# Optimization experiments

Hardware: AMD Instinct MI355X
Metric: run time of the kernel (lower is better)

Reference implementation:

```python
import jax, jax.numpy as jnp
import numpy as np
import jax.scipy.linalg as jsp

H = 8
C = 64
D_CONV = 4
EPS_L2 = 1e-6
EPS_RMS = 1e-5


def l2norm(x):
    return x * jax.lax.rsqrt(jnp.sum(x * x, axis=-1, keepdims=True) + EPS_L2)


def setup_inputs() -> dict:
    key = jax.random.key(0)
    ks = jax.random.split(key, 12)
    B, T, D = 4, 4096, 1024
    x = jax.random.normal(ks[0], (B, T, D), dtype=jnp.float32)
    s = 0.02
    Wv = jax.random.normal(ks[1], (D, D), dtype=jnp.float32) * s
    Wg = jax.random.normal(ks[2], (D, D), dtype=jnp.float32) * s
    Wo = jax.random.normal(ks[3], (D, D), dtype=jnp.float32) * s
    Wb = jax.random.normal(ks[4], (H, D), dtype=jnp.float32) * s
    Wa = jax.random.normal(ks[5], (H, D), dtype=jnp.float32) * s
    # dt_bias / A_log initialized as in the torch module
    u = jax.random.uniform(ks[6], (H,))
    dt = jnp.exp(u * (jnp.log(0.1) - jnp.log(0.001)) + jnp.log(0.001))
    dt_bias = dt + jnp.log(-jnp.expm1(-dt))
    A_log = jnp.log(jax.random.uniform(ks[7], (H,)) * 16.0 + 1e-4)
    norm_w = jnp.ones((D // H,), dtype=jnp.float32)
    conv_w = jax.random.normal(ks[8], (D, D_CONV), dtype=jnp.float32) * 0.1
    conv_b = jnp.zeros((D,), dtype=jnp.float32)
    return {"x": x, "Wv": Wv, "Wg": Wg, "Wo": Wo, "Wb": Wb, "Wa": Wa,
            "dt_bias": dt_bias, "A_log": A_log, "norm_w": norm_w,
            "conv_w": conv_w, "conv_b": conv_b}


def _causal_depthwise_conv(x, w, b):
    # x: (B,T,D), w: (D,d_conv) -- causal depthwise conv1d
    B, T, D = x.shape
    xp = jnp.pad(x, ((0, 0), (D_CONV - 1, 0), (0, 0)))
    out = b
    for j in range(D_CONV):
        out = out + xp[:, j:j + T] * w[:, j]
    return out


def _forward(x, Wv, Wg, Wo, Wb, Wa, dt_bias, A_log, norm_w, conv_w, conv_b):
    B, T, D = x.shape
    K = D // H
    n = T // C  # T chosen as a multiple of C, so pad_len == 0

    rk = l2norm(x.reshape(B, T, H, K)) / np.sqrt(K)
    x_shift = jnp.pad(x[:, :-1], ((0, 0), (1, 0), (0, 0)))
    wk = l2norm(x_shift.reshape(B, T, H, K))
    v = jax.nn.silu(_causal_depthwise_conv(x @ Wv.T, conv_w, conv_b)).reshape(B, T, H, K)
    gate = (x @ Wg.T).reshape(B, T, H, K)
    beta = jax.nn.sigmoid(x @ Wb.T)                       # (B,T,H)
    decay = -jnp.exp(A_log) * jax.nn.softplus(x @ Wa.T + dt_bias)  # (B,T,H)

    # -> (B,H,T,K)
    rk, wk, v = (jnp.transpose(t, (0, 2, 1, 3)) for t in (rk, wk, v))
    beta_t = jnp.transpose(beta, (0, 2, 1))[..., None]    # (B,H,T,1)
    v = v * beta_t
    wk_beta = wk * beta_t

    # chunk: (B,H,n,C,K)
    ch = lambda t: t.reshape(B, H, n, C, K)
    rk, wk, v, wk_beta = ch(rk), ch(wk), ch(v), ch(wk_beta)
    decay = jnp.cumsum(jnp.transpose(decay, (0, 2, 1)).reshape(B, H, n, C), axis=-1)
    decay_exp = jnp.exp(decay)[..., None]                 # (B,H,n,C,1)

    tril = jnp.tril(jnp.ones((C, C), dtype=bool))
    strict_lower = jnp.tril(jnp.ones((C, C), dtype=bool), k=-1)
    diff = decay[..., :, None] - decay[..., None, :]
    L_mask = jnp.where(tril, jnp.exp(jnp.where(tril, diff, 0.0)), 0.0)  # (B,H,n,C,C)

    A_strict = jnp.where(strict_lower,
                         -(jnp.einsum('bhnck,bhndk->bhncd', wk_beta, wk) * L_mask), 0.0)
    # forward-substitution loop == inverse of unit-lower-triangular (I - A_strict)
    eye = jnp.eye(C, dtype=x.dtype)
    Tmat = jsp.solve_triangular(eye - A_strict,
                                jnp.broadcast_to(eye, A_strict.shape),
                                lower=True)
    v = Tmat @ v
    wk_cumdecay = Tmat @ (wk_beta * decay_exp)

    # scan over chunks maintaining state S: (B,H,K,K)
    def step(S, inp):
        rk_i, wk_i, v_i, wkc_i, L_i, dec_i = inp
        attn = jnp.where(tril, jnp.einsum('bhck,bhdk->bhcd', rk_i, wk_i) * L_i, 0.0)
        v_new = v_i - wkc_i @ S
        o_inter = (rk_i * jnp.exp(dec_i)[..., None]) @ S
        o_i = o_inter + attn @ v_new
        dw = jnp.exp(dec_i[..., -1:] - dec_i)[..., None]
        S_new = S * jnp.exp(dec_i[..., -1])[..., None, None] + \
            jnp.einsum('bhck,bhcv->bhkv', wk_i * dw, v_new)
        return S_new, o_i

    mv = lambda t: jnp.moveaxis(t, 2, 0)  # chunk axis to front
    S0 = jnp.zeros((B, H, K, K), dtype=x.dtype)
    _, o = jax.lax.scan(step, S0, (mv(rk), mv(wk), mv(v), mv(wk_cumdecay),
                                   mv(L_mask), mv(decay)))
    # o: (n,B,H,C,K) -> (B,T,H,K)
    o = jnp.transpose(o, (1, 0, 3, 2, 4)).reshape(B, T, H, K)

    # per-head RMSNorm, gated, output projection
    o = o * jax.lax.rsqrt(jnp.mean(o * o, axis=-1, keepdims=True) + EPS_RMS) * norm_w
    o = o * jax.nn.silu(gate)
    return o.reshape(B, T, D) @ Wo.T


def reference(x, Wv, Wg, Wo, Wb, Wa, dt_bias, A_log, norm_w, conv_w, conv_b):
    return _forward(x, Wv, Wg, Wo, Wb, Wa, dt_bias, A_log, norm_w, conv_w, conv_b)
```

## Files before the change

### kernel.cpp

```cpp
#include <hip/hip_runtime.h>
#include <hip/hip_bf16.h>
#include <math.h>

#define H_ 8
#define K_ 128
#define C_ 64
#define D_ 1024
#define T_ 4096
#define B_ 4
#define N_CH 64
#define BT_ (B_*T_)

typedef __attribute__((ext_vector_type(8))) short bf16x8;
typedef __attribute__((ext_vector_type(4))) float f32x4;
typedef __hip_bfloat16 bf16;

#define BAR_LGKM() do { \
  asm volatile("s_waitcnt lgkmcnt(0)" ::: "memory"); \
  __builtin_amdgcn_sched_barrier(0); \
  __builtin_amdgcn_s_barrier(); \
} while(0)

__device__ __forceinline__ float siluf(float x){ return x / (1.0f + expf(-x)); }
__device__ __forceinline__ float expn(float x){ return expf(fminf(x, 0.f)); }
__device__ __forceinline__ float sanf(float v){ return (__builtin_fabsf(v) <= 1e30f) ? v : 0.f; }

__device__ __forceinline__ void ld_bf4(const bf16* p, float* o){
  uint2 u = *(const uint2*)p;
  o[0]=__uint_as_float(u.x<<16); o[1]=__uint_as_float(u.x&0xffff0000u);
  o[2]=__uint_as_float(u.y<<16); o[3]=__uint_as_float(u.y&0xffff0000u);
}
__device__ __forceinline__ void ld_bf4s(const bf16* p, float* o){
  ld_bf4(p, o);
#pragma unroll
  for (int e=0;e<4;e++) o[e] = sanf(o[e]);
}
__device__ __forceinline__ unsigned short f2bfu(float f){
  bf16 h = __float2bfloat16(f);
  return *reinterpret_cast<unsigned short*>(&h);
}
__device__ __forceinline__ uint2 pack_bf4(const float* v){
  uint2 r;
  r.x = (unsigned)f2bfu(v[0]) | ((unsigned)f2bfu(v[1])<<16);
  r.y = (unsigned)f2bfu(v[2]) | ((unsigned)f2bfu(v[3])<<16);
  return r;
}
__device__ __forceinline__ bf16x8 u4_to_b8(uint4 u){
  union { uint4 u; bf16x8 b; } cv; cv.u = u; return cv.b;
}

template<int I> __device__ __forceinline__ void fsub_step(float* v, const float (*sa)[64]){
  const float* ar = sa[I];
  float s0=0.f,s1=0.f,s2=0.f,s3=0.f;
  constexpr int I4 = I & ~3;
#pragma unroll
  for (int j=0;j<I4;j+=4){
    float4 a4 = *(const float4*)&ar[j];
    s0 += a4.x*v[j+0]; s1 += a4.y*v[j+1]; s2 += a4.z*v[j+2]; s3 += a4.w*v[j+3];
  }
#pragma unroll
  for (int j=I4;j<I;j++) s0 += ar[j]*v[j];
  v[I] += (s0+s2)+(s1+s3);
}
template<int I> __device__ __forceinline__ void fsub_all(float* v, const float (*sa)[64]){
  if constexpr (I >= 1){
    fsub_all<I-1>(v, sa);
    fsub_step<I>(v, sa);
  }
}

__global__ __launch_bounds__(256) void cast_f2b(
    const float* __restrict__ src, bf16* __restrict__ dst, int n4)
{
  int i = blockIdx.x*256 + threadIdx.x;
  if (i >= n4) return;
  float4 v = *(const float4*)&src[(size_t)i*4];
  float a[4] = {v.x, v.y, v.z, v.w};
  *(uint2*)&dst[(size_t)i*4] = pack_bf4(a);
}

template<typename OUT_T, bool FUSE_NG>
__global__ __launch_bounds__(256) void gemm_bt_mfma(
    const bf16* __restrict__ X, const bf16* __restrict__ W,
    OUT_T* __restrict__ Y, int M, int N, int K,
    const bf16* __restrict__ o_in, const float* __restrict__ norm_w)
{
  __shared__ __align__(16) bf16 As[128*64];
  __shared__ __align__(16) bf16 Bs[128*64];
  const int tid = threadIdx.x;
  const int wv = tid >> 6;
  const int lane = tid & 63;
  const int row0 = blockIdx.y*128, col0 = blockIdx.x*128;
  const int mw = (wv&1)*64, nw = (wv>>1)*64;
  const int q = lane >> 4;
  const int l15 = lane & 15;
  const int swr = l15 & 7;
  f32x4 acc[4][4];
#pragma unroll
  for (int mi=0;mi<4;mi++)
#pragma unroll
    for (int ni=0;ni<4;ni++) acc[mi][ni] = (f32x4){0.f,0.f,0.f,0.f};

  const int sr8 = lane >> 3;
  const int scs = ((lane & 7) ^ sr8) * 8;
  for (int k0=0;k0<K;k0+=64){
#pragma unroll
    for (int i=0;i<4;i++){
      __builtin_amdgcn_global_load_lds(
          (const void*)&X[(size_t)(row0 + i*32 + wv*8 + sr8)*K + k0 + scs],
          (void*)&As[i*2048 + wv*512], 16, 0, 0);
      __builtin_amdgcn_global_load_lds(
          (const void*)&W[(size_t)(col0 + i*32 + wv*8 + sr8)*K + k0 + scs],
          (void*)&Bs[i*2048 + wv*512], 16, 0, 0);
    }
    __syncthreads();
#pragma unroll
    for (int ks=0; ks<64; ks+=32){
      bf16x8 af[4], bfr[4];
#pragma unroll
      for (int i=0;i<4;i++){
        const int cc = (((ks>>3) + q) ^ swr) * 8;
        af[i]  = *(const bf16x8*)&As[(mw + i*16 + l15)*64 + cc];
        bfr[i] = *(const bf16x8*)&Bs[(nw + i*16 + l15)*64 + cc];
      }
#pragma unroll
      for (int mi=0;mi<4;mi++)
#pragma unroll
        for (int ni=0;ni<4;ni++)
          acc[mi][ni] = __builtin_amdgcn_mfma_f32_16x16x32_bf16(af[mi], bfr[ni], acc[mi][ni], 0,0,0);
    }
    __syncthreads();
  }

  if constexpr (FUSE_NG){
    float* s_red = (float*)As;
    const int hh = blockIdx.x;
    const int nwh = nw >> 6;
#pragma unroll
    for (int mi=0;mi<4;mi++){
#pragma unroll
      for (int reg=0;reg<4;reg++){
        int row = row0 + mw + mi*16 + q*4 + reg;
        int b = row >> 12, t = row & (T_-1);
        const bf16* orow = o_in + ((size_t)(b*H_+hh)*T_ + t)*K_;
        float ps = 0.f;
#pragma unroll
        for (int ni=0;ni<4;ni++){
          float ov = sanf(__bfloat162float(orow[nw + ni*16 + l15]));
          ps += ov*ov;
        }
        ps += __shfl_xor(ps,1,64); ps += __shfl_xor(ps,2,64);
        ps += __shfl_xor(ps,4,64); ps += __shfl_xor(ps,8,64);
        if (l15 == 0) s_red[nwh*128 + mw + mi*16 + q*4 + reg] = ps;
      }
    }
    __syncthreads();
#pragma unroll
    for (int mi=0;mi<4;mi++){
#pragma unroll
      for (int reg=0;reg<4;reg++){
        int lr = mw + mi*16 + q*4 + reg;
        float ssum = s_red[lr] + s_red[128 + lr];
        float rr = rsqrtf(ssum*(1.f/128.f) + 1e-5f);
        int row = row0 + lr;
        int b = row >> 12, t = row & (T_-1);
        const bf16* orow = o_in + ((size_t)(b*H_+hh)*T_ + t)*K_;
#pragma unroll
        for (int ni=0;ni<4;ni++){
          int k = nw + ni*16 + l15;
          float ov = sanf(__bfloat162float(orow[k]));
          float res = ov * rr * norm_w[k] * siluf(acc[mi][ni][reg]);
          Y[(size_t)row*N + col0 + k] = (OUT_T)__float2bfloat16(res);
        }
      }
    }
  } else {
#pragma unroll
    for (int mi=0;mi<4;mi++){
#pragma unroll
      for (int reg=0;reg<4;reg++){
        int row = row0 + mw + mi*16 + q*4 + reg;
#pragma unroll
        for (int ni=0;ni<4;ni++){
          int col = col0 + nw + ni*16 + l15;
          if constexpr (sizeof(OUT_T) == 2)
            Y[(size_t)row*N + col] = (OUT_T)__float2bfloat16(acc[mi][ni][reg]);
          else
            Y[(size_t)row*N + col] = (OUT_T)acc[mi][ni][reg];
        }
      }
    }
  }
}

__global__ __launch_bounds__(256) void proj_small(
    const float* __restrict__ x, const float* __restrict__ Wb, const float* __restrict__ Wa,
    const float* __restrict__ dt_bias, const float* __restrict__ A_log,
    float* __restrict__ beta_out, float* __restrict__ dec_out)
{
  const int w = threadIdx.x >> 6;
  const int lane = threadIdx.x & 63;
  const int bt = blockIdx.x*4 + w;
  const int b = bt >> 12, t = bt & (T_-1);
  const float* xr = x + (size_t)bt*D_;
  float xv[16];
#pragma unroll
  for (int p=0;p<4;p++){
    float4 v = *(const float4*)&xr[lane*16 + p*4];
    xv[p*4+0]=v.x; xv[p*4+1]=v.y; xv[p*4+2]=v.z; xv[p*4+3]=v.w;
  }
  float accb[H_], acca[H_];
#pragma unroll
  for (int h=0;h<H_;h++){
    float sb=0.f, sa=0.f;
#pragma unroll
    for (int p=0;p<4;p++){
      float4 wb = *(const float4*)&Wb[(size_t)h*D_ + lane*16 + p*4];
      float4 wa = *(const float4*)&Wa[(size_t)h*D_ + lane*16 + p*4];
      sb += xv[p*4+0]*wb.x + xv[p*4+1]*wb.y + xv[p*4+2]*wb.z + xv[p*4+3]*wb.w;
      sa += xv[p*4+0]*wa.x + xv[p*4+1]*wa.y + xv[p*4+2]*wa.z + xv[p*4+3]*wa.w;
    }
    accb[h]=sb; acca[h]=sa;
  }
#pragma unroll
  for (int h=0;h<H_;h++){
#pragma unroll
    for (int m=1;m<64;m<<=1){
      accb[h] += __shfl_xor(accb[h], m, 64);
      acca[h] += __shfl_xor(acca[h], m, 64);
    }
  }
  if (lane < H_) {
    int h = lane;
    beta_out[(size_t)(b*H_+h)*T_ + t] = 1.f/(1.f+expf(-accb[h]));
  } else if (lane < 2*H_) {
    int h = lane - H_;
    float z = acca[h] + dt_bias[h];
    float sp = fmaxf(z,0.f) + log1pf(expf(-fabsf(z)));
    dec_out[(size_t)(b*H_+h)*T_ + t] = -expf(A_log[h]) * sp;
  }
}

__global__ __launch_bounds__(256) void xinv_kernel(
    const float* __restrict__ x, float* __restrict__ xinv, bf16* __restrict__ xb)
{
  const int bt = blockIdx.x;
  const int b = bt >> 12, t = bt & (T_-1);
  const int tid = threadIdx.x;
  float4 xv = *(const float4*)&x[(size_t)bt*D_ + tid*4];
  float a[4] = {xv.x, xv.y, xv.z, xv.w};
  *(uint2*)&xb[(size_t)bt*D_ + tid*4] = pack_bf4(a);
  float ss = xv.x*xv.x + xv.y*xv.y + xv.z*xv.z + xv.w*xv.w;
#pragma unroll
  for (int m=1;m<32;m<<=1) ss += __shfl_xor(ss, m, 32);
  const int h = tid >> 5;
  if ((tid & 31) == 0)
    xinv[(size_t)(b*H_+h)*T_ + t] = rsqrtf(ss + 1e-6f);
}

__global__ __launch_bounds__(256) void cumsum_dec(
    const float* __restrict__ dec_raw, float* __restrict__ dec_cum)
{
  int g = blockIdx.x*4 + (threadIdx.x>>6);
  int lane = threadIdx.x & 63;
  float v = sanf(dec_raw[(size_t)g*C_ + lane]);
#pragma unroll
  for (int off=1; off<64; off<<=1){
    float u = __shfl_up(v, off, 64);
    if (lane >= off) v += u;
  }
  dec_cum[(size_t)g*C_ + lane] = v;
}

__global__ __launch_bounds__(256) void chunk_prep(
    const bf16* __restrict__ xb, const float* __restrict__ xinv,
    const bf16* __restrict__ vpre, const float* __restrict__ cw, const float* __restrict__ cb,
    const float* __restrict__ beta, const float* __restrict__ dec,
    bf16* __restrict__ vchk, bf16* __restrict__ wkc, bf16* __restrict__ attn)
{
  __shared__ __align__(16) bf16 s_x[65][136];
  __shared__ __align__(16) float s_a[64][64];
  __shared__ float s_dec[64], s_beta[64], s_invsh[64], s_negbi[64], s_rsc[64], s_sc2[64];

  const int tid = threadIdx.x;
  const int chunk = blockIdx.x;
  const int bh = chunk >> 6;
  const int nc = chunk & 63;
  const int b = bh >> 3, h = bh & 7;
  const int t0 = nc * C_;
  const size_t xrow = (size_t)b*T_;
  const size_t rowb = (size_t)bh*T_ + t0;
  const size_t kobase = rowb * K_;
  const int w = tid >> 6;
  const int lane = tid & 63;
  const int l15 = lane & 15;
  const int q = lane >> 4;

  for (int idx = tid; idx < 65*16; idx += 256){
    int r = idx >> 4;
    int seg = (idx & 15) * 8;
    int t = t0 + r - 1;
    int tr = t < 0 ? 0 : t;
    *(uint4*)&s_x[r][seg] = *(const uint4*)&xb[(xrow + tr)*D_ + h*K_ + seg];
  }
  if (tid < C_){
    int c = tid;
    float dv  = sanf(dec[rowb + c]);
    float bet = sanf(beta[rowb + c]);
    float invc = sanf(xinv[rowb + c]);
    int tm1 = t0 + c - 1;
    float ivs = (tm1 >= 0) ? sanf(xinv[(size_t)bh*T_ + tm1]) : 0.f;
    s_dec[c] = dv;
    s_beta[c] = bet;
    s_invsh[c] = ivs;
    s_negbi[c] = -bet * ivs;
    s_rsc[c] = invc * 0.08838834764831845f;
    s_sc2[c] = ivs * bet * expn(dv);
  }
  __syncthreads();

  bf16x8 aG[4], aT[4];
#pragma unroll
  for (int ks=0; ks<4; ks++){
    aG[ks] = *(const bf16x8*)&s_x[16*w + l15][ks*32 + q*8];
    aT[ks] = *(const bf16x8*)&s_x[16*w + l15 + 1][ks*32 + q*8];
  }
  f32x4 accG[4], accT[4];
#pragma unroll
  for (int J=0;J<4;J++){ accG[J]=(f32x4){0.f,0.f,0.f,0.f}; accT[J]=(f32x4){0.f,0.f,0.f,0.f}; }
#pragma unroll
  for (int J=0;J<4;J++){
    if (J <= w){
#pragma unroll
      for (int ks=0; ks<4; ks++){
        bf16x8 bfrag = *(const bf16x8*)&s_x[16*J + l15][ks*32 + q*8];
        accG[J] = __builtin_amdgcn_mfma_f32_16x16x32_bf16(aG[ks], bfrag, accG[J], 0,0,0);
        accT[J] = __builtin_amdgcn_mfma_f32_16x16x32_bf16(aT[ks], bfrag, accT[J], 0,0,0);
      }
    }
  }
  {
    const int i0 = 16*w + q*4;
#pragma unroll
    for (int J=0;J<4;J++){
      const int j = 16*J + l15;
#pragma unroll
      for (int reg=0;reg<4;reg++){
        const int i = i0 + reg;
        if (j < i)
          s_a[i][j] = s_negbi[i] * s_invsh[j] * expn(s_dec[i]-s_dec[j]) * accG[J][reg];
        float val = 0.f;
        if (j <= i)
          val = s_rsc[i] * s_invsh[j] * expn(s_dec[i]-s_dec[j]) * accT[J][reg];
        attn[(size_t)chunk*4096 + i*64 + j] = __float2bfloat16(val);
      }
    }
  }

  float v[64];
  if (tid < 128){
    const int col = tid;
    float4 cwv = *(const float4*)&cw[(h*K_+col)*4];
    const float cbv = cb[h*K_+col];
    const bf16* vp = vpre + (xrow + t0)*D_ + h*K_ + col;
    float win0, win1, win2;
    { int t = t0-3; win0 = (t>=0)? sanf(__bfloat162float(vpre[(xrow+t)*D_+h*K_+col])) : 0.f; }
    { int t = t0-2; win1 = (t>=0)? sanf(__bfloat162float(vpre[(xrow+t)*D_+h*K_+col])) : 0.f; }
    { int t = t0-1; win2 = (t>=0)? sanf(__bfloat162float(vpre[(xrow+t)*D_+h*K_+col])) : 0.f; }
#pragma unroll
    for (int c8=0; c8<8; c8++){
      float nv[8];
#pragma unroll
      for (int u=0;u<8;u++) nv[u] = sanf(__bfloat162float(vp[(size_t)(c8*8+u)*D_]));
#pragma unroll
      for (int u=0;u<8;u++){
        const int c = c8*8+u;
        float a = cbv + cwv.x*win0 + cwv.y*win1 + cwv.z*win2 + cwv.w*nv[u];
        v[c] = siluf(a) * s_beta[c];
        win0=win1; win1=win2; win2=nv[u];
      }
    }
  } else {
    const int col = tid - 128;
#pragma unroll
    for (int c=0;c<64;c++)
      v[c] = __bfloat162float(s_x[c][col]) * s_sc2[c];
  }
  __syncthreads();

  fsub_all<63>(v, s_a);

  {
    const int col = tid & 127;
    bf16* dst = (tid < 128 ? vchk : wkc) + kobase + col;
#pragma unroll
    for (int c=0;c<64;c++)
      dst[(size_t)c*K_] = __float2bfloat16(v[c]);
  }
}

__global__ __launch_bounds__(256) void scan_kernel(
    const bf16* __restrict__ xb, const float* __restrict__ xinv, bf16* vo,
    const bf16* __restrict__ wkc, const bf16* __restrict__ attn,
    const float* __restrict__ dec)
{
  __shared__ __align__(16) bf16 xst[2][128][72];
  __shared__ __align__(16) bf16 st_hi[16][136];
  __shared__ __align__(16) bf16 st_lo[16][136];
  __shared__ __align__(16) bf16 vn_t [16][72];
  __shared__ __align__(16) bf16 vn_sh[16][72];
  __shared__ __align__(16) bf16 vn_sl[16][72];

  const int tid = threadIdx.x;
  const int bh = blockIdx.x & 31;
  const int g  = blockIdx.x >> 5;
  const int b = bh >> 3, h = bh & 7;
  const int j0 = g*16;
  const int w  = tid >> 6;
  const int lane = tid & 63;
  const int l15 = lane & 15;
  const int q = lane >> 4;
  const int wrow = 16*w;
  const int c0 = wrow + q*4;
  const size_t xrow = (size_t)b*T_;
  const size_t bhT = (size_t)bh*T_;

  for (int e=tid; e<16*136; e+=256){
    ((unsigned short*)&st_hi[0][0])[e] = 0;
    ((unsigned short*)&st_lo[0][0])[e] = 0;
  }

  const int xc0 = (tid & 31)*2;
  const int xkb = (tid >> 5)*16;

  f32x4 accS[2];
  accS[0] = (f32x4){0.f,0.f,0.f,0.f};
  accS[1] = (f32x4){0.f,0.f,0.f,0.f};

  uint4 T_r[4];
  uint4 P_w[4], P_x[4], P_a[2];
  bf16  P_v[4];
  float4 P_d, P_xi;
  float P_d63, P_xm[4];

  auto issue_t = [&](int c){
    int t0 = c*C_;
    int t1 = t0 + xc0 - 1;
    const bf16* p1 = xb + (xrow + (t1<0?0:t1))*D_ + h*K_ + xkb;
    const bf16* p2 = xb + (xrow + (t0+xc0))*D_ + h*K_ + xkb;
    T_r[0]=*(const uint4*)p1; T_r[1]=*(const uint4*)(p1+8);
    T_r[2]=*(const uint4*)p2; T_r[3]=*(const uint4*)(p2+8);
  };
  auto write_xst = [&](int buf){
    unsigned r1[8]={T_r[0].x,T_r[0].y,T_r[0].z,T_r[0].w,T_r[1].x,T_r[1].y,T_r[1].z,T_r[1].w};
    unsigned r2[8]={T_r[2].x,T_r[2].y,T_r[2].z,T_r[2].w,T_r[3].x,T_r[3].y,T_r[3].z,T_r[3].w};
#pragma unroll
    for (int i2=0;i2<8;i2++){
      *(unsigned*)&xst[buf][xkb + 2*i2][xc0]     = (r1[i2] & 0xffffu) | (r2[i2] << 16);
      *(unsigned*)&xst[buf][xkb + 2*i2 + 1][xc0] = (r1[i2] >> 16) | (r2[i2] & 0xffff0000u);
    }
  };
  auto issue_main = [&](int c){
    int t0 = c*C_;
    size_t rowb = bhT + t0;
    const bf16* pw = wkc + (rowb + wrow + l15)*K_ + q*8;
    const bf16* px = xb + (xrow + t0 + wrow + l15)*D_ + h*K_ + q*8;
#pragma unroll
    for (int ks=0; ks<4; ks++){
      P_w[ks] = *(const uint4*)(pw + ks*32);
      P_x[ks] = *(const uint4*)(px + ks*32);
    }
    const bf16* pv = vo + (rowb + c0)*K_ + j0 + l15;
#pragma unroll
    for (int r=0;r<4;r++) P_v[r] = pv[(size_t)r*K_];
    P_d   = *(const float4*)&dec[rowb + c0];
    P_d63 = dec[rowb + 63];
    P_xi  = *(const float4*)&xinv[bhT + t0 + c0];
#pragma unroll
    for (int r=0;r<4;r++){
      int tm1 = t0 + c0 + r - 1;
      P_xm[r] = (tm1 >= 0) ? xinv[bhT + tm1] : 0.f;
    }
  };
  auto issue_att = [&](int c){
    const bf16* pa = attn + (size_t)(bh*N_CH + c)*4096 + (wrow + l15)*64 + q*8;
    P_a[0] = *(const uint4*)pa;
    P_a[1] = *(const uint4*)(pa + 32);
  };

  issue_t(0);
  write_xst(0);
  issue_t(1);
  issue_main(0);
  issue_att(0);
  BAR_LGKM();

  for (int nc=0; nc<N_CH; nc++){
    const int t0 = nc*C_;
    const size_t rowb = bhT + t0;

    float d63s = sanf(P_d63);
    float a63 = expn(d63s);
    float cdA[4] = {sanf(P_d.x), sanf(P_d.y), sanf(P_d.z), sanf(P_d.w)};
    float cxiA[4] = {sanf(P_xi.x), sanf(P_xi.y), sanf(P_xi.z), sanf(P_xi.w)};
    float sov[4], scv[4], vinitf[4];
#pragma unroll
    for (int r=0;r<4;r++){
      sov[r] = cxiA[r] * 0.08838834764831845f * expn(cdA[r]);
      scv[r] = sanf(P_xm[r]) * expn(d63s - cdA[r]);
      vinitf[r] = __bfloat162float(P_v[r]);
    }

    write_xst((nc+1)&1);
    issue_t(nc+2 < N_CH ? nc+2 : N_CH-1);

    f32x4 accV, accP = (f32x4){0.f,0.f,0.f,0.f};
#pragma unroll
    for (int r=0;r<4;r++) accV[r] = vinitf[r];
    __builtin_amdgcn_s_setprio(1);
#pragma unroll
    for (int ks=0; ks<4; ks++){
      bf16x8 bh_ = *(const bf16x8*)&st_hi[l15][ks*32 + q*8];
      bf16x8 bl_ = *(const bf16x8*)&st_lo[l15][ks*32 + q*8];
      uint4 uw = P_w[ks];
      uw.x ^= 0x80008000u; uw.y ^= 0x80008000u; uw.z ^= 0x80008000u; uw.w ^= 0x80008000u;
      bf16x8 a1 = u4_to_b8(uw);
      bf16x8 a2 = u4_to_b8(P_x[ks]);
      accV = __builtin_amdgcn_mfma_f32_16x16x32_bf16(a1, bh_, accV, 0,0,0);
      accV = __builtin_amdgcn_mfma_f32_16x16x32_bf16(a1, bl_, accV, 0,0,0);
      accP = __builtin_amdgcn_mfma_f32_16x16x32_bf16(a2, bh_, accP, 0,0,0);
      accP = __builtin_amdgcn_mfma_f32_16x16x32_bf16(a2, bl_, accP, 0,0,0);
    }
    __builtin_amdgcn_s_setprio(0);
    f32x4 oacc;
#pragma unroll
    for (int r=0;r<4;r++) oacc[r] = accP[r] * sov[r];
    {
      float v4[4] = {accV[0],accV[1],accV[2],accV[3]};
      *(uint2*)&vn_t[l15][c0] = pack_bf4(v4);
      float vs[4];
#pragma unroll
      for (int r=0;r<4;r++) vs[r] = accV[r] * scv[r];
      uint2 ph = pack_bf4(vs);
      float lo4[4];
      lo4[0] = vs[0] - __uint_as_float(ph.x << 16);
      lo4[1] = vs[1] - __uint_as_float(ph.x & 0xffff0000u);
      lo4[2] = vs[2] - __uint_as_float(ph.y << 16);
      lo4[3] = vs[3] - __uint_as_float(ph.y & 0xffff0000u);
      *(uint2*)&vn_sh[l15][c0] = ph;
      *(uint2*)&vn_sl[l15][c0] = pack_bf4(lo4);
    }
    issue_main(nc+1 < N_CH ? nc+1 : N_CH-1);
    BAR_LGKM();

    __builtin_amdgcn_s_setprio(1);
#pragma unroll
    for (int ks=0; ks<2; ks++){
      bf16x8 bV = *(const bf16x8*)&vn_t[l15][ks*32 + q*8];
      bf16x8 aA = u4_to_b8(P_a[ks]);
      oacc = __builtin_amdgcn_mfma_f32_16x16x32_bf16(aA, bV, oacc, 0,0,0);
    }
    __builtin_amdgcn_s_setprio(0);
    {
      bf16* po = vo + (rowb + c0)*K_ + j0 + l15;
#pragma unroll
      for (int r=0;r<4;r++) po[(size_t)r*K_] = __float2bfloat16(oacc[r]);
    }
    issue_att(nc+1 < N_CH ? nc+1 : N_CH-1);
    __builtin_amdgcn_s_setprio(1);
    {
      bf16x8 aH[2], aL[2];
#pragma unroll
      for (int ks=0; ks<2; ks++){
        aH[ks] = *(const bf16x8*)&vn_sh[l15][ks*32 + q*8];
        aL[ks] = *(const bf16x8*)&vn_sl[l15][ks*32 + q*8];
      }
#pragma unroll
      for (int sub=0; sub<2; sub++){
        f32x4 acc = accS[sub];
#pragma unroll
        for (int r=0;r<4;r++) acc[r] *= a63;
#pragma unroll
        for (int ks=0; ks<2; ks++){
          bf16x8 bX = *(const bf16x8*)&xst[nc&1][32*w + 16*sub + l15][ks*32 + q*8];
          acc = __builtin_amdgcn_mfma_f32_16x16x32_bf16(aH[ks], bX, acc, 0,0,0);
          acc = __builtin_amdgcn_mfma_f32_16x16x32_bf16(aL[ks], bX, acc, 0,0,0);
        }
        accS[sub] = acc;
#pragma unroll
        for (int r=0;r<4;r++){
          float sv = acc[r];
          bf16 hb = __float2bfloat16(sv);
          st_hi[q*4+r][32*w + 16*sub + l15] = hb;
          st_lo[q*4+r][32*w + 16*sub + l15] = __float2bfloat16(sv - __bfloat162float(hb));
        }
      }
    }
    __builtin_amdgcn_s_setprio(0);
    BAR_LGKM();
  }
}

extern "C" void kernel_launch(void* const* d_in, const int* in_sizes, int n_in,
                              void* d_out, int out_size, void* d_ws, size_t ws_size,
                              hipStream_t stream)
{
  const float* x       = (const float*)d_in[0];
  const float* Wv      = (const float*)d_in[1];
  const float* Wg      = (const float*)d_in[2];
  const float* Wo      = (const float*)d_in[3];
  const float* Wb      = (const float*)d_in[4];
  const float* Wa      = (const float*)d_in[5];
  const float* dt_bias = (const float*)d_in[6];
  const float* A_log   = (const float*)d_in[7];
  const float* norm_w  = (const float*)d_in[8];
  const float* conv_w  = (const float*)d_in[9];
  const float* conv_b  = (const float*)d_in[10];
  float* out = (float*)d_out;

  const size_t BTD = (size_t)B_*T_*D_;
  const size_t BHT = (size_t)B_*H_*T_;
  const size_t DD  = (size_t)D_*D_;

  float* beta = (float*)d_ws;
  float* decr = beta + BHT;
  float* decc = decr + BHT;
  float* xinv = decc + BHT;
  bf16* Wvb = (bf16*)(xinv + BHT);
  bf16* Wgb = Wvb + DD;
  bf16* Wob = Wgb + DD;
  bf16* xb   = Wob + DD;
  bf16* vpre = xb + BTD;
  bf16* wkc  = vpre + BTD;
  bf16* vo   = (bf16*)d_out;
  bf16* attn = vo + BTD;

  dim3 gemm_grid(D_/128, BT_/128);
  xinv_kernel<<<BT_, 256, 0, stream>>>(x, xinv, xb);
  cast_f2b<<<(DD/4+255)/256, 256, 0, stream>>>(Wv, Wvb, DD/4);
  cast_f2b<<<(DD/4+255)/256, 256, 0, stream>>>(Wg, Wgb, DD/4);
  cast_f2b<<<(DD/4+255)/256, 256, 0, stream>>>(Wo, Wob, DD/4);
  gemm_bt_mfma<bf16,false><<<gemm_grid, 256, 0, stream>>>(xb, Wvb, vpre, BT_, D_, D_, nullptr, nullptr);
  proj_small<<<BT_/4, 256, 0, stream>>>(x, Wb, Wa, dt_bias, A_log, beta, decr);
  cumsum_dec<<<(BHT/C_)/4, 256, 0, stream>>>(decr, decc);
  chunk_prep<<<B_*H_*N_CH, 256, 0, stream>>>(xb, xinv, vpre, conv_w, conv_b,
                                             beta, decc, vo , wkc, attn);
  scan_kernel<<<B_*H_*8, 256, 0, stream>>>(xb, xinv, vo, wkc, attn, decc);
  gemm_bt_mfma<bf16,true><<<gemm_grid, 256, 0, stream>>>(xb, Wgb, vpre, BT_, D_, D_, vo, norm_w);
  gemm_bt_mfma<float,false><<<gemm_grid, 256, 0, stream>>>(vpre, Wob, out, BT_, D_, D_, nullptr, nullptr);
}
```

Baseline: 618.9 us.

## Warp-specialize scan kernel into state-recurrence and output/staging wave groups

The scan kernel now runs 512 threads per block. Waves 0-3 run only the serial state recurrence: the v_new MFMAs, the hi/lo split and the state update. Waves 4-7 stage the transposed x tile into shared memory, prefetch x, attn, decay and xinv, and compute the inter-chunk and intra-chunk outputs and their stores. The aim is to take the output GEMMs and global loads off the serial chunk-to-chunk path so they overlap with the recurrence. The cost is twice as many waves per block, more registers and occupancy pressure, and a barrier protocol that must keep both groups in lockstep.

```diff
diff --git a/kernel.cpp b/kernel.cpp
--- a/kernel.cpp
+++ b/kernel.cpp
@@ -399,7 +399,7 @@
   }
 }
 
-__global__ __launch_bounds__(256) void scan_kernel(
+__global__ __launch_bounds__(512) void scan_kernel(
     const bf16* __restrict__ xb, const float* __restrict__ xinv, bf16* vo,
     const bf16* __restrict__ wkc, const bf16* __restrict__ attn,
     const float* __restrict__ dec)
@@ -417,158 +417,98 @@
   const int b = bh >> 3, h = bh & 7;
   const int j0 = g*16;
   const int w  = tid >> 6;
+  const int wm = w & 3;
   const int lane = tid & 63;
   const int l15 = lane & 15;
   const int q = lane >> 4;
-  const int wrow = 16*w;
+  const int wrow = 16*wm;
   const int c0 = wrow + q*4;
   const size_t xrow = (size_t)b*T_;
   const size_t bhT = (size_t)bh*T_;
 
-  for (int e=tid; e<16*136; e+=256){
+  for (int e=tid; e<16*136; e+=512){
     ((unsigned short*)&st_hi[0][0])[e] = 0;
     ((unsigned short*)&st_lo[0][0])[e] = 0;
   }
 
-  const int xc0 = (tid & 31)*2;
-  const int xkb = (tid >> 5)*16;
-
-  f32x4 accS[2];
-  accS[0] = (f32x4){0.f,0.f,0.f,0.f};
-  accS[1] = (f32x4){0.f,0.f,0.f,0.f};
-
-  uint4 T_r[4];
-  uint4 P_w[4], P_x[4], P_a[2];
-  bf16  P_v[4];
-  float4 P_d, P_xi;
-  float P_d63, P_xm[4];
-
-  auto issue_t = [&](int c){
-    int t0 = c*C_;
-    int t1 = t0 + xc0 - 1;
-    const bf16* p1 = xb + (xrow + (t1<0?0:t1))*D_ + h*K_ + xkb;
-    const bf16* p2 = xb + (xrow + (t0+xc0))*D_ + h*K_ + xkb;
-    T_r[0]=*(const uint4*)p1; T_r[1]=*(const uint4*)(p1+8);
-    T_r[2]=*(const uint4*)p2; T_r[3]=*(const uint4*)(p2+8);
-  };
-  auto write_xst = [&](int buf){
-    unsigned r1[8]={T_r[0].x,T_r[0].y,T_r[0].z,T_r[0].w,T_r[1].x,T_r[1].y,T_r[1].z,T_r[1].w};
-    unsigned r2[8]={T_r[2].x,T_r[2].y,T_r[2].z,T_r[2].w,T_r[3].x,T_r[3].y,T_r[3].z,T_r[3].w};
-#pragma unroll
-    for (int i2=0;i2<8;i2++){
-      *(unsigned*)&xst[buf][xkb + 2*i2][xc0]     = (r1[i2] & 0xffffu) | (r2[i2] << 16);
-      *(unsigned*)&xst[buf][xkb + 2*i2 + 1][xc0] = (r1[i2] >> 16) | (r2[i2] & 0xffff0000u);
-    }
-  };
-  auto issue_main = [&](int c){
-    int t0 = c*C_;
-    size_t rowb = bhT + t0;
-    const bf16* pw = wkc + (rowb + wrow + l15)*K_ + q*8;
-    const bf16* px = xb + (xrow + t0 + wrow + l15)*D_ + h*K_ + q*8;
-#pragma unroll
-    for (int ks=0; ks<4; ks++){
-      P_w[ks] = *(const uint4*)(pw + ks*32);
-      P_x[ks] = *(const uint4*)(px + ks*32);
-    }
-    const bf16* pv = vo + (rowb + c0)*K_ + j0 + l15;
+  if (w < 4){
+    f32x4 accS[2];
+    accS[0] = (f32x4){0.f,0.f,0.f,0.f};
+    accS[1] = (f32x4){0.f,0.f,0.f,0.f};
+
+    const bf16*  pw   = wkc + (bhT + wrow + l15)*K_ + q*8;
+    const bf16*  pv   = vo  + (bhT + c0)*K_ + j0 + l15;
+    const float* pd   = dec + bhT + c0;
+    const float* pd63 = dec + bhT + 63;
+    const float* pxm  = xinv + bhT + c0;
+
+    uint4 P_w[4]; bf16 P_v[4]; float4 P_d; float P_d63, P_xm[4];
+#pragma unroll
+    for (int ks=0; ks<4; ks++) P_w[ks] = *(const uint4*)(pw + ks*32);
 #pragma unroll
     for (int r=0;r<4;r++) P_v[r] = pv[(size_t)r*K_];
-    P_d   = *(const float4*)&dec[rowb + c0];
-    P_d63 = dec[rowb + 63];
-    P_xi  = *(const float4*)&xinv[bhT + t0 + c0];
+    P_d = *(const float4*)pd;
+    P_d63 = *pd63;
 #pragma unroll
     for (int r=0;r<4;r++){
-      int tm1 = t0 + c0 + r - 1;
+      int tm1 = c0 + r - 1;
       P_xm[r] = (tm1 >= 0) ? xinv[bhT + tm1] : 0.f;
     }
-  };
-  auto issue_att = [&](int c){
-    const bf16* pa = attn + (size_t)(bh*N_CH + c)*4096 + (wrow + l15)*64 + q*8;
-    P_a[0] = *(const uint4*)pa;
-    P_a[1] = *(const uint4*)(pa + 32);
-  };
-
-  issue_t(0);
-  write_xst(0);
-  issue_t(1);
-  issue_main(0);
-  issue_att(0);
-  BAR_LGKM();
-
-  for (int nc=0; nc<N_CH; nc++){
-    const int t0 = nc*C_;
-    const size_t rowb = bhT + t0;
-
-    float d63s = sanf(P_d63);
-    float a63 = expn(d63s);
-    float cdA[4] = {sanf(P_d.x), sanf(P_d.y), sanf(P_d.z), sanf(P_d.w)};
-    float cxiA[4] = {sanf(P_xi.x), sanf(P_xi.y), sanf(P_xi.z), sanf(P_xi.w)};
-    float sov[4], scv[4], vinitf[4];
-#pragma unroll
-    for (int r=0;r<4;r++){
-      sov[r] = cxiA[r] * 0.08838834764831845f * expn(cdA[r]);
-      scv[r] = sanf(P_xm[r]) * expn(d63s - cdA[r]);
-      vinitf[r] = __bfloat162float(P_v[r]);
-    }
-
-    write_xst((nc+1)&1);
-    issue_t(nc+2 < N_CH ? nc+2 : N_CH-1);
-
-    f32x4 accV, accP = (f32x4){0.f,0.f,0.f,0.f};
-#pragma unroll
-    for (int r=0;r<4;r++) accV[r] = vinitf[r];
-    __builtin_amdgcn_s_setprio(1);
-#pragma unroll
-    for (int ks=0; ks<4; ks++){
-      bf16x8 bh_ = *(const bf16x8*)&st_hi[l15][ks*32 + q*8];
-      bf16x8 bl_ = *(const bf16x8*)&st_lo[l15][ks*32 + q*8];
-      uint4 uw = P_w[ks];
-      uw.x ^= 0x80008000u; uw.y ^= 0x80008000u; uw.z ^= 0x80008000u; uw.w ^= 0x80008000u;
-      bf16x8 a1 = u4_to_b8(uw);
-      bf16x8 a2 = u4_to_b8(P_x[ks]);
-      accV = __builtin_amdgcn_mfma_f32_16x16x32_bf16(a1, bh_, accV, 0,0,0);
-      accV = __builtin_amdgcn_mfma_f32_16x16x32_bf16(a1, bl_, accV, 0,0,0);
-      accP = __builtin_amdgcn_mfma_f32_16x16x32_bf16(a2, bh_, accP, 0,0,0);
-      accP = __builtin_amdgcn_mfma_f32_16x16x32_bf16(a2, bl_, accP, 0,0,0);
-    }
-    __builtin_amdgcn_s_setprio(0);
-    f32x4 oacc;
-#pragma unroll
-    for (int r=0;r<4;r++) oacc[r] = accP[r] * sov[r];
-    {
-      float v4[4] = {accV[0],accV[1],accV[2],accV[3]};
-      *(uint2*)&vn_t[l15][c0] = pack_bf4(v4);
-      float vs[4];
-#pragma unroll
-      for (int r=0;r<4;r++) vs[r] = accV[r] * scv[r];
-      uint2 ph = pack_bf4(vs);
-      float lo4[4];
-      lo4[0] = vs[0] - __uint_as_float(ph.x << 16);
-      lo4[1] = vs[1] - __uint_as_float(ph.x & 0xffff0000u);
-      lo4[2] = vs[2] - __uint_as_float(ph.y << 16);
-      lo4[3] = vs[3] - __uint_as_float(ph.y & 0xffff0000u);
-      *(uint2*)&vn_sh[l15][c0] = ph;
-      *(uint2*)&vn_sl[l15][c0] = pack_bf4(lo4);
-    }
-    issue_main(nc+1 < N_CH ? nc+1 : N_CH-1);
     BAR_LGKM();
 
-    __builtin_amdgcn_s_setprio(1);
-#pragma unroll
-    for (int ks=0; ks<2; ks++){
-      bf16x8 bV = *(const bf16x8*)&vn_t[l15][ks*32 + q*8];
-      bf16x8 aA = u4_to_b8(P_a[ks]);
-      oacc = __builtin_amdgcn_mfma_f32_16x16x32_bf16(aA, bV, oacc, 0,0,0);
-    }
-    __builtin_amdgcn_s_setprio(0);
-    {
-      bf16* po = vo + (rowb + c0)*K_ + j0 + l15;
-#pragma unroll
-      for (int r=0;r<4;r++) po[(size_t)r*K_] = __float2bfloat16(oacc[r]);
-    }
-    issue_att(nc+1 < N_CH ? nc+1 : N_CH-1);
-    __builtin_amdgcn_s_setprio(1);
-    {
+    for (int nc=0; nc<N_CH; nc++){
+      float d63s = sanf(P_d63);
+      float a63 = expn(d63s);
+      float cd[4] = {sanf(P_d.x), sanf(P_d.y), sanf(P_d.z), sanf(P_d.w)};
+      float scv[4], vinitf[4];
+#pragma unroll
+      for (int r=0;r<4;r++){
+        scv[r] = sanf(P_xm[r]) * expn(d63s - cd[r]);
+        vinitf[r] = __bfloat162float(P_v[r]);
+      }
+
+      f32x4 accV;
+#pragma unroll
+      for (int r=0;r<4;r++) accV[r] = vinitf[r];
+      __builtin_amdgcn_s_setprio(1);
+#pragma unroll
+      for (int ks=0; ks<4; ks++){
+        bf16x8 bh_ = *(const bf16x8*)&st_hi[l15][ks*32 + q*8];
+        bf16x8 bl_ = *(const bf16x8*)&st_lo[l15][ks*32 + q*8];
+        uint4 uw = P_w[ks];
+        uw.x ^= 0x80008000u; uw.y ^= 0x80008000u; uw.z ^= 0x80008000u; uw.w ^= 0x80008000u;
+        bf16x8 a1 = u4_to_b8(uw);
+        accV = __builtin_amdgcn_mfma_f32_16x16x32_bf16(a1, bh_, accV, 0,0,0);
+        accV = __builtin_amdgcn_mfma_f32_16x16x32_bf16(a1, bl_, accV, 0,0,0);
+      }
+      __builtin_amdgcn_s_setprio(0);
+      {
+        float v4[4] = {accV[0],accV[1],accV[2],accV[3]};
+        *(uint2*)&vn_t[l15][c0] = pack_bf4(v4);
+        float vs[4];
+#pragma unroll
+        for (int r=0;r<4;r++) vs[r] = accV[r] * scv[r];
+        uint2 ph = pack_bf4(vs);
+        float lo4[4];
+        lo4[0] = vs[0] - __uint_as_float(ph.x << 16);
+        lo4[1] = vs[1] - __uint_as_float(ph.x & 0xffff0000u);
+        lo4[2] = vs[2] - __uint_as_float(ph.y << 16);
+        lo4[3] = vs[3] - __uint_as_float(ph.y & 0xffff0000u);
+        *(uint2*)&vn_sh[l15][c0] = ph;
+        *(uint2*)&vn_sl[l15][c0] = pack_bf4(lo4);
+      }
+      if (nc+1 < N_CH){ pw += (size_t)C_*K_; pv += (size_t)C_*K_; pd += C_; pd63 += C_; pxm += C_; }
+#pragma unroll
+      for (int ks=0; ks<4; ks++) P_w[ks] = *(const uint4*)(pw + ks*32);
+#pragma unroll
+      for (int r=0;r<4;r++) P_v[r] = pv[(size_t)r*K_];
+      P_d = *(const float4*)pd;
+      P_d63 = *pd63;
+#pragma unroll
+      for (int r=0;r<4;r++) P_xm[r] = pxm[r-1];
+      BAR_LGKM();
+
+      __builtin_amdgcn_s_setprio(1);
       bf16x8 aH[2], aL[2];
 #pragma unroll
       for (int ks=0; ks<2; ks++){
@@ -582,7 +522,7 @@
         for (int r=0;r<4;r++) acc[r] *= a63;
 #pragma unroll
         for (int ks=0; ks<2; ks++){
-          bf16x8 bX = *(const bf16x8*)&xst[nc&1][32*w + 16*sub + l15][ks*32 + q*8];
+          bf16x8 bX = *(const bf16x8*)&xst[nc&1][32*wm + 16*sub + l15][ks*32 + q*8];
           acc = __builtin_amdgcn_mfma_f32_16x16x32_bf16(aH[ks], bX, acc, 0,0,0);
           acc = __builtin_amdgcn_mfma_f32_16x16x32_bf16(aL[ks], bX, acc, 0,0,0);
         }
@@ -591,13 +531,119 @@
         for (int r=0;r<4;r++){
           float sv = acc[r];
           bf16 hb = __float2bfloat16(sv);
-          st_hi[q*4+r][32*w + 16*sub + l15] = hb;
-          st_lo[q*4+r][32*w + 16*sub + l15] = __float2bfloat16(sv - __bfloat162float(hb));
+          st_hi[q*4+r][32*wm + 16*sub + l15] = hb;
+          st_lo[q*4+r][32*wm + 16*sub + l15] = __float2bfloat16(sv - __bfloat162float(hb));
         }
       }
-    }
-    __builtin_amdgcn_s_setprio(0);
+      __builtin_amdgcn_s_setprio(0);
+      BAR_LGKM();
+    }
+  } else {
+    const int tp = tid - 256;
+    const int xc0 = (tp & 31)*2;
+    const int xkb = (tp >> 5)*16;
+
+    uint4 T_r[4];
+    uint4 P_x[4], P_a[2];
+    float4 P_dP, P_xi;
+
+    {
+      int t1 = xc0 - 1;
+      const bf16* p1 = xb + (xrow + (t1<0?0:t1))*D_ + h*K_ + xkb;
+      const bf16* p2 = xb + (xrow + xc0)*D_ + h*K_ + xkb;
+      T_r[0]=*(const uint4*)p1; T_r[1]=*(const uint4*)(p1+8);
+      T_r[2]=*(const uint4*)p2; T_r[3]=*(const uint4*)(p2+8);
+    }
+    {
+      unsigned r1[8]={T_r[0].x,T_r[0].y,T_r[0].z,T_r[0].w,T_r[1].x,T_r[1].y,T_r[1].z,T_r[1].w};
+      unsigned r2[8]={T_r[2].x,T_r[2].y,T_r[2].z,T_r[2].w,T_r[3].x,T_r[3].y,T_r[3].z,T_r[3].w};
+#pragma unroll
+      for (int i2=0;i2<8;i2++){
+        *(unsigned*)&xst[0][xkb + 2*i2][xc0]     = (r1[i2] & 0xffffu) | (r2[i2] << 16);
+        *(unsigned*)&xst[0][xkb + 2*i2 + 1][xc0] = (r1[i2] >> 16) | (r2[i2] & 0xffff0000u);
+      }
+    }
+    {
+      const bf16* p1 = xb + (xrow + C_ + xc0 - 1)*D_ + h*K_ + xkb;
+      const bf16* p2 = xb + (xrow + C_ + xc0)*D_ + h*K_ + xkb;
+      T_r[0]=*(const uint4*)p1; T_r[1]=*(const uint4*)(p1+8);
+      T_r[2]=*(const uint4*)p2; T_r[3]=*(const uint4*)(p2+8);
+    }
+    const bf16* pt1 = xb + (xrow + 2*C_ + xc0 - 1)*D_ + h*K_ + xkb;
+    const bf16* pt2 = xb + (xrow + 2*C_ + xc0)*D_ + h*K_ + xkb;
+
+    const bf16*  px  = xb + (xrow + wrow + l15)*D_ + h*K_ + q*8;
+    const bf16*  pa  = attn + (size_t)(bh*N_CH)*4096 + (wrow + l15)*64 + q*8;
+    const float* pdP = dec + bhT + c0;
+    const float* pxi = xinv + bhT + c0;
+    bf16*        pvo = vo + (bhT + c0)*K_ + j0 + l15;
+
+#pragma unroll
+    for (int ks=0; ks<4; ks++) P_x[ks] = *(const uint4*)(px + ks*32);
+    P_a[0] = *(const uint4*)pa; P_a[1] = *(const uint4*)(pa + 32);
+    P_dP = *(const float4*)pdP;
+    P_xi = *(const float4*)pxi;
     BAR_LGKM();
+
+    for (int nc=0; nc<N_CH; nc++){
+      float cd[4]  = {sanf(P_dP.x), sanf(P_dP.y), sanf(P_dP.z), sanf(P_dP.w)};
+      float cxi[4] = {sanf(P_xi.x), sanf(P_xi.y), sanf(P_xi.z), sanf(P_xi.w)};
+      float sov[4];
+#pragma unroll
+      for (int r=0;r<4;r++) sov[r] = cxi[r] * 0.08838834764831845f * expn(cd[r]);
+
+      {
+        unsigned r1[8]={T_r[0].x,T_r[0].y,T_r[0].z,T_r[0].w,T_r[1].x,T_r[1].y,T_r[1].z,T_r[1].w};
+        unsigned r2[8]={T_r[2].x,T_r[2].y,T_r[2].z,T_r[2].w,T_r[3].x,T_r[3].y,T_r[3].z,T_r[3].w};
+        const int buf = (nc+1)&1;
+#pragma unroll
+        for (int i2=0;i2<8;i2++){
+          *(unsigned*)&xst[buf][xkb + 2*i2][xc0]     = (r1[i2] & 0xffffu) | (r2[i2] << 16);
+          *(unsigned*)&xst[buf][xkb + 2*i2 + 1][xc0] = (r1[i2] >> 16) | (r2[i2] & 0xffff0000u);
+        }
+      }
+      if (nc+2 < N_CH){
+        T_r[0]=*(const uint4*)pt1; T_r[1]=*(const uint4*)(pt1+8);
+        T_r[2]=*(const uint4*)pt2; T_r[3]=*(const uint4*)(pt2+8);
+        pt1 += (size_t)C_*D_; pt2 += (size_t)C_*D_;
+      }
+
+      f32x4 accP = (f32x4){0.f,0.f,0.f,0.f};
+      __builtin_amdgcn_s_setprio(1);
+#pragma unroll
+      for (int ks=0; ks<4; ks++){
+        bf16x8 bh_ = *(const bf16x8*)&st_hi[l15][ks*32 + q*8];
+        bf16x8 bl_ = *(const bf16x8*)&st_lo[l15][ks*32 + q*8];
+        bf16x8 a2 = u4_to_b8(P_x[ks]);
+        accP = __builtin_amdgcn_mfma_f32_16x16x32_bf16(a2, bh_, accP, 0,0,0);
+        accP = __builtin_amdgcn_mfma_f32_16x16x32_bf16(a2, bl_, accP, 0,0,0);
+      }
+      __builtin_amdgcn_s_setprio(0);
+      f32x4 oacc;
+#pragma unroll
+      for (int r=0;r<4;r++) oacc[r] = accP[r] * sov[r];
+      if (nc+1 < N_CH){ px += (size_t)C_*D_; pdP += C_; pxi += C_; }
+#pragma unroll
+      for (int ks=0; ks<4; ks++) P_x[ks] = *(const uint4*)(px + ks*32);
+      P_dP = *(const float4*)pdP;
+      P_xi = *(const float4*)pxi;
+      BAR_LGKM();
+
+      __builtin_amdgcn_s_setprio(1);
+#pragma unroll
+      for (int ks=0; ks<2; ks++){
+        bf16x8 bV = *(const bf16x8*)&vn_t[l15][ks*32 + q*8];
+        bf16x8 aA = u4_to_b8(P_a[ks]);
+        oacc = __builtin_amdgcn_mfma_f32_16x16x32_bf16(aA, bV, oacc, 0,0,0);
+      }
+      __builtin_amdgcn_s_setprio(0);
+#pragma unroll
+      for (int r=0;r<4;r++) pvo[(size_t)r*K_] = __float2bfloat16(oacc[r]);
+      pvo += (size_t)C_*K_;
+      if (nc+1 < N_CH){ pa += 4096; }
+      P_a[0] = *(const uint4*)pa; P_a[1] = *(const uint4*)(pa + 32);
+      BAR_LGKM();
+    }
   }
 }
 
@@ -645,7 +691,7 @@
   cumsum_dec<<<(BHT/C_)/4, 256, 0, stream>>>(decr, decc);
   chunk_prep<<<B_*H_*N_CH, 256, 0, stream>>>(xb, xinv, vpre, conv_w, conv_b,
                                              beta, decc, vo , wkc, attn);
-  scan_kernel<<<B_*H_*8, 256, 0, stream>>>(xb, xinv, vo, wkc, attn, decc);
+  scan_kernel<<<B_*H_*8, 512, 0, stream>>>(xb, xinv, vo, wkc, attn, decc);
   gemm_bt_mfma<bf16,true><<<gemm_grid, 256, 0, stream>>>(xb, Wgb, vpre, BT_, D_, D_, vo, norm_w);
   gemm_bt_mfma<float,false><<<gemm_grid, 256, 0, stream>>>(vpre, Wob, out, BT_, D_, D_, nullptr, nullptr);
 }
```

New measurement: 586.9 us. 5.2% less time.
